# Performance work log

Hardware: AMD Instinct MI355X
Metric: run time of the kernel (lower is better)

The kernel has to match this reference:

```python
import jax, jax.numpy as jnp
import numpy as np

S = 64        # state_size (nodes per graph == feature width)
B = 1024      # number of graphs
N = B * S     # total nodes
DEG = 16      # avg degree
E = N * DEG   # total edges
A = 16        # attractors
EPS = 1e-5


def setup_inputs() -> dict:
    key = jax.random.key(0)
    ks = jax.random.split(key, 16)
    x = jax.random.normal(ks[0], (N, 1), dtype=jnp.float32)
    # block-diagonal batched graphs: each graph has S nodes, S*DEG edges
    epg = S * DEG
    gid = jnp.arange(E, dtype=jnp.int32) // epg
    src = gid * S + jax.random.randint(ks[1], (E,), 0, S, dtype=jnp.int32)
    dst = gid * S + jax.random.randint(ks[2], (E,), 0, S, dtype=jnp.int32)
    edge_index = jnp.stack([src, dst], axis=0)
    f32 = jnp.float32
    return {
        "x": x, "edge_index": edge_index,
        # EdgeConv MLP: Linear(2,4) -> ReLU -> Linear(4,S)
        "w1": jax.random.normal(ks[3], (2, 4), f32) * 0.5,
        "b1": jnp.zeros((4,), f32),
        "w2": jax.random.normal(ks[4], (4, S), f32) * 0.3,
        "b2": jnp.zeros((S,), f32),
        # Conv1d(S,S,3,padding=1) x2
        "conv2_w": jax.random.normal(ks[5], (S, S, 3), f32) / np.sqrt(3 * S),
        "conv2_b": jnp.zeros((S,), f32),
        "conv3_w": jax.random.normal(ks[6], (S, S, 3), f32) / np.sqrt(3 * S),
        "conv3_b": jnp.zeros((S,), f32),
        # BatchNorm affine params
        "g1": jnp.ones((S,), f32), "be1": jnp.zeros((S,), f32),
        "g2": jnp.ones((S,), f32), "be2": jnp.zeros((S,), f32),
        "g3": jnp.ones((S,), f32), "be3": jnp.zeros((S,), f32),
        # MLP tail
        "wm1": jax.random.normal(ks[7], (S * S, 256), f32) / np.sqrt(S * S),
        "bm1": jnp.zeros((256,), f32),
        "wm2": jax.random.normal(ks[8], (256, 256), f32) / 16.0,
        "bm2": jnp.zeros((256,), f32),
        "wm3": jax.random.normal(ks[9], (256, 256), f32) / 16.0,
        "bm3": jnp.zeros((256,), f32),
        "wp": jax.random.normal(ks[10], (256, A), f32) / 16.0,
        "bp": jnp.zeros((A,), f32),
    }


def _bn(h, gamma, beta, axes):
    # training-mode batch norm (biased variance), per-channel
    mean = jnp.mean(h, axis=axes, keepdims=True)
    var = jnp.mean(jnp.square(h - mean), axis=axes, keepdims=True)
    inv = jax.lax.rsqrt(var + EPS)
    sh = [1] * h.ndim
    sh[1] = -1
    return (h - mean) * inv * gamma.reshape(sh) + beta.reshape(sh)


def _conv1d(h, w, b):
    # h: [B, C, L], w: [O, I, K], padding=1 -> same length
    out = jax.lax.conv_general_dilated(
        h, w, window_strides=(1,), padding=((1, 1),),
        dimension_numbers=("NCH", "OIH", "NCH"))
    return out + b[None, :, None]


def reference(x, edge_index, w1, b1, w2, b2, conv2_w, conv2_b, conv3_w, conv3_b,
              g1, be1, g2, be2, g3, be3, wm1, bm1, wm2, bm2, wm3, bm3, wp, bp):
    src, dst = edge_index[0], edge_index[1]
    # EdgeConv (aggr='add'): nn(cat[x_i, x_j - x_i]) summed at target i
    xi = x[dst]                              # [E,1] gather
    xj = x[src]                              # [E,1] gather
    m = jnp.concatenate([xi, xj - xi], axis=-1)      # [E,2]
    m = jax.nn.relu(m @ w1 + b1)                     # [E,4]
    m = m @ w2 + b2                                   # [E,S]
    out = jax.ops.segment_sum(m, dst, num_segments=N)  # [N,S] scatter-add
    # BN1 + ReLU on [N,S] (channel dim = 1)
    out = jax.nn.relu(_bn(out, g1, be1, axes=(0,)))
    # per-graph feature map: [B, S_nodes, S_feat] -> channels-first [B,S,S]
    out = out.reshape(B, S, S).swapaxes(1, 2)
    out = jax.nn.relu(_bn(_conv1d(out, conv2_w, conv2_b), g2, be2, axes=(0, 2)))
    out = jax.nn.relu(_bn(_conv1d(out, conv3_w, conv3_b), g3, be3, axes=(0, 2)))
    out = out.reshape(B, S * S)
    out = jax.nn.relu(out @ wm1 + bm1)
    out = jax.nn.relu(out @ wm2 + bm2)
    out = jax.nn.relu(out @ wm3 + bm3)
    logits = out @ wp + bp                            # [B, A]
    return jax.nn.log_softmax(logits, axis=1)
```

## Files before the change

### kernel.cpp

```cpp
#include <hip/hip_runtime.h>
#include <cstdint>
#include <cstddef>

typedef __attribute__((ext_vector_type(8))) short short8;
typedef __attribute__((ext_vector_type(8))) unsigned short ushort8;
typedef __attribute__((ext_vector_type(4))) float f32x4;

#define EPSV 1e-5f
#define NB 1024
#define NEDGE 1048576
#define EPG 1024
#define CNTF 65536.0f
#define REP 32

__device__ __forceinline__ ushort f2bf(float f) {
  uint u = __float_as_uint(f);
  return (ushort)((u + 0x7FFFu + ((u >> 16) & 1u)) >> 16);
}
__device__ __forceinline__ float bf2f(ushort u) {
  return __uint_as_float((uint)u << 16);
}

__global__ __launch_bounds__(256) void k_prepw(
    const float* __restrict__ wm1, const float* __restrict__ wm2,
    const float* __restrict__ wm3, const float* __restrict__ wp,
    const float* __restrict__ c2w, const float* __restrict__ c3w,
    ushort* __restrict__ wbf1t, ushort* __restrict__ wbf2t,
    ushort* __restrict__ wbf3t, ushort* __restrict__ wptbf,
    ushort* __restrict__ cwt2, ushort* __restrict__ cwt3,
    float* __restrict__ stats)
{
  __shared__ ushort T[64][72];
  const int tid = threadIdx.x;
  const int bb = blockIdx.x;

  if (bb < 256) {
    const int kc = bb >> 2, n0 = (bb & 3) << 6;
    const int kk = tid >> 2, np = (tid & 3) << 4;
    const float* srow = wm1 + (((size_t)(kk << 6) + kc) << 8) + n0 + np;
#pragma unroll
    for (int i = 0; i < 4; ++i) {
      const float4 v = *(const float4*)(srow + (i << 2));
      const int n = np + (i << 2);
      T[n + 0][kk] = f2bf(v.x); T[n + 1][kk] = f2bf(v.y);
      T[n + 2][kk] = f2bf(v.z); T[n + 3][kk] = f2bf(v.w);
    }
    __syncthreads();
    ushort* dst = wbf1t + ((size_t)kc << 14) + (n0 << 6);
    const int nl = tid >> 2, qk = (tid & 3) << 4;
    *(ushort8*)(dst + (nl << 6) + qk) = *(ushort8*)&T[nl][qk];
    *(ushort8*)(dst + (nl << 6) + qk + 8) = *(ushort8*)&T[nl][qk + 8];
    return;
  }
  if (bb < 320) {
    const int base = (((bb - 256) << 8) + tid) << 3;
    const int m = base >> 16;
    const int rem = base & 65535;
    const int kc = rem >> 14, within = rem & 16383;
    const int n = within >> 6, kk0 = within & 63;
    const float* src = m ? wm3 : wm2;
    ushort* dst = m ? wbf3t : wbf2t;
    ushort tmp[8];
#pragma unroll
    for (int j = 0; j < 8; ++j)
      tmp[j] = f2bf(src[(((kc << 6) | (kk0 + j)) << 8) + n]);
    *(ushort8*)&dst[rem] = *(ushort8*)&tmp[0];
    return;
  }
  if (bb == 320) {
    const int a = tid & 15, k0 = (tid >> 4) << 4;
    ushort tmp[16];
#pragma unroll
    for (int j = 0; j < 16; ++j) tmp[j] = f2bf(wp[((k0 + j) << 4) + a]);
    *(ushort8*)&wptbf[(a << 8) + k0] = *(ushort8*)&tmp[0];
    *(ushort8*)&wptbf[(a << 8) + k0 + 8] = *(ushort8*)&tmp[8];
    return;
  }
  if (bb == 417) {
    float4 z4 = make_float4(0.f, 0.f, 0.f, 0.f);
#pragma unroll
    for (int i = 0; i < 12; ++i) ((float4*)stats)[(i << 8) + tid] = z4;
    return;
  }
  const int flat = (bb - 321) * 256 + tid;
  const int m = flat >= 12288;
  const int idx = flat - (m ? 12288 : 0);
  const float* src = m ? c3w : c2w;
  ushort* dst = m ? cwt3 : cwt2;
  const int o = idx / 192, rem = idx - o * 192;
  const int kk = rem >> 6, c = rem & 63;
  dst[idx] = f2bf(src[o * 192 + c * 3 + kk]);
}

__global__ __launch_bounds__(256) void k_edge(
    const float* __restrict__ x, const int* __restrict__ ei,
    const float* __restrict__ w1, const float* __restrict__ b1,
    const float* __restrict__ w2, const float* __restrict__ b2,
    ushort* __restrict__ out0, float* __restrict__ stats1)
{
  __shared__ float xs[64];
  __shared__ float aggT[4][5][72];
  __shared__ float aggC[64][8];
  __shared__ float w1s[8], b1s[4];
  __shared__ float w2s[256], b2s[64];
  __shared__ float rs[4][64], rss[4][64];
  const int tid = threadIdx.x;
  const int b = blockIdx.x;
  const int w = tid >> 6;

  if (tid < 8) w1s[tid] = w1[tid];
  if (tid < 4) b1s[tid] = b1[tid];
  if (tid < 64) { xs[tid] = x[(b << 6) + tid]; b2s[tid] = b2[tid]; }
  w2s[tid] = w2[tid];
  for (int i = tid; i < 1440; i += 256) ((float*)aggT)[i] = 0.f;
  __syncthreads();

  const int e0 = b * EPG;
  const int4 s4 = ((const int4*)(ei + e0))[tid];
  const int4 d4 = ((const int4*)(ei + NEDGE + e0))[tid];
  float* agw = &aggT[w][0][0];
  const int sls[4] = {s4.x & 63, s4.y & 63, s4.z & 63, s4.w & 63};
  const int dls[4] = {d4.x & 63, d4.y & 63, d4.z & 63, d4.w & 63};
#pragma unroll
  for (int e = 0; e < 4; ++e) {
    const int dl = dls[e];
    const float xi = xs[dl];
    const float dx = xs[sls[e]] - xi;
#pragma unroll
    for (int j = 0; j < 4; ++j) {
      float h = fmaxf(fmaf(xi, w1s[j], fmaf(dx, w1s[4 + j], b1s[j])), 0.f);
      atomicAdd(&agw[j * 72 + dl], h);
    }
    atomicAdd(&agw[4 * 72 + dl], 1.0f);
  }
  __syncthreads();

  if (tid < 64) {
    const int n = tid;
    const float a0 = aggT[0][0][n] + aggT[1][0][n] + aggT[2][0][n] + aggT[3][0][n];
    const float a1 = aggT[0][1][n] + aggT[1][1][n] + aggT[2][1][n] + aggT[3][1][n];
    const float a2 = aggT[0][2][n] + aggT[1][2][n] + aggT[2][2][n] + aggT[3][2][n];
    const float a3v = aggT[0][3][n] + aggT[1][3][n] + aggT[2][3][n] + aggT[3][3][n];
    const float dg = aggT[0][4][n] + aggT[1][4][n] + aggT[2][4][n] + aggT[3][4][n];
    *(float4*)&aggC[n][0] = make_float4(a0, a1, a2, a3v);
    aggC[n][4] = dg;
  }
  __syncthreads();

  const int c = tid & 63, qq = tid >> 6;
  const float wc0 = w2s[c], wc1 = w2s[64 + c], wc2 = w2s[128 + c], wc3 = w2s[192 + c];
  const float b2c = b2s[c];
  float s = 0.f, ss = 0.f;
  for (int n = qq; n < 64; n += 4) {
    const float4 a = *(const float4*)&aggC[n][0];
    const float dg = aggC[n][4];
    float v = a.x * wc0 + a.y * wc1 + a.z * wc2 + a.w * wc3 + dg * b2c;
    out0[(size_t)(((b << 6) + n) << 6) + c] = f2bf(v);
    s += v; ss += v * v;
  }
  rs[qq][c] = s; rss[qq][c] = ss;
  __syncthreads();
  if (tid < 64) {
    float* dst = stats1 + ((b & (REP - 1)) << 7);
    atomicAdd(&dst[tid], rs[0][tid] + rs[1][tid] + rs[2][tid] + rs[3][tid]);
    atomicAdd(&dst[64 + tid], rss[0][tid] + rss[1][tid] + rss[2][tid] + rss[3][tid]);
  }
}

__global__ __launch_bounds__(256) void k_convm(
    const ushort* __restrict__ in,
    const float* __restrict__ stats_in,
    const float* __restrict__ gamma, const float* __restrict__ beta,
    const ushort* __restrict__ cwt, const float* __restrict__ cb,
    ushort* __restrict__ out,
    float* __restrict__ stats_out)
{
  __shared__ ushort As[64][200];
  __shared__ ushort Yt[66][72];
  __shared__ float aco[64], bco[64], cbs[64];
  __shared__ float ldsS[64], ldsSS[64];
  const int tid = threadIdx.x;
  const int b = blockIdx.x;

  if (tid < 64) {
    float sm = 0.f, sq = 0.f;
#pragma unroll 8
    for (int r = 0; r < REP; ++r) {
      sm += stats_in[(r << 7) + tid];
      sq += stats_in[(r << 7) + 64 + tid];
    }
    const float mean = sm * (1.0f / CNTF);
    const float var = sq * (1.0f / CNTF) - mean * mean;
    const float a = gamma[tid] * rsqrtf(var + EPSV);
    aco[tid] = a;
    bco[tid] = beta[tid] - mean * a;
    cbs[tid] = cb[tid];
    Yt[0][tid] = 0;
    Yt[65][tid] = 0;
  }
  __syncthreads();

  const size_t base = (size_t)b << 12;
  {
    const int lr = tid >> 2, p = (tid & 3) << 4;
    const ushort8 r0 = *(const ushort8*)&in[base + (lr << 6) + p];
    const ushort8 r1 = *(const ushort8*)&in[base + (lr << 6) + p + 8];
    ushort tmp[16];
#pragma unroll
    for (int j = 0; j < 8; ++j)
      tmp[j] = f2bf(fmaxf(fmaf(aco[p + j], bf2f(r0[j]), bco[p + j]), 0.f));
#pragma unroll
    for (int j = 0; j < 8; ++j)
      tmp[8 + j] = f2bf(fmaxf(fmaf(aco[p + 8 + j], bf2f(r1[j]), bco[p + 8 + j]), 0.f));
    *(ushort8*)&Yt[lr + 1][p] = *(ushort8*)&tmp[0];
    *(ushort8*)&Yt[lr + 1][p + 8] = *(ushort8*)&tmp[8];
  }
  {
    const ushort8* gw = (const ushort8*)cwt;
#pragma unroll
    for (int i = 0; i < 6; ++i) {
      const int e8 = (i << 8) + tid;
      const int o = e8 / 24, k8 = (e8 - o * 24) << 3;
      *(ushort8*)&As[o][k8] = gw[e8];
    }
  }
  __syncthreads();

  const int lane = tid & 63, w = tid >> 6;
  const int lm = lane & 15, q = lane >> 4;
  f32x4 acc[4];
#pragma unroll
  for (int nt = 0; nt < 4; ++nt) acc[nt] = (f32x4){0.f, 0.f, 0.f, 0.f};

#pragma unroll
  for (int kk = 0; kk < 3; ++kk) {
#pragma unroll
    for (int ks = 0; ks < 2; ++ks) {
      const short8 af = *(const short8*)&As[(w << 4) + lm][(kk << 6) + (ks << 5) + (q << 3)];
#pragma unroll
      for (int nt = 0; nt < 4; ++nt) {
        const short8 bfr = *(const short8*)&Yt[(nt << 4) + lm + kk][(ks << 5) + (q << 3)];
        acc[nt] = __builtin_amdgcn_mfma_f32_16x16x32_bf16(af, bfr, acc[nt], 0, 0, 0);
      }
    }
  }

  const int obase = (w << 4) + (q << 2);
  const float4 cb4 = *(const float4*)&cbs[obase];
  float s[4] = {0.f, 0.f, 0.f, 0.f}, ss[4] = {0.f, 0.f, 0.f, 0.f};
#pragma unroll
  for (int nt = 0; nt < 4; ++nt) {
    const int l = (nt << 4) + lm;
    float4 v = make_float4(acc[nt][0] + cb4.x, acc[nt][1] + cb4.y,
                           acc[nt][2] + cb4.z, acc[nt][3] + cb4.w);
    *(ushort4*)&out[base + (l << 6) + obase] =
        make_ushort4(f2bf(v.x), f2bf(v.y), f2bf(v.z), f2bf(v.w));
    s[0] += v.x; ss[0] += v.x * v.x;
    s[1] += v.y; ss[1] += v.y * v.y;
    s[2] += v.z; ss[2] += v.z * v.z;
    s[3] += v.w; ss[3] += v.w * v.w;
  }
#pragma unroll
  for (int i = 0; i < 4; ++i) {
#pragma unroll
    for (int off = 1; off < 16; off <<= 1) {
      s[i] += __shfl_xor(s[i], off);
      ss[i] += __shfl_xor(ss[i], off);
    }
    if (lm == 0) { ldsS[obase + i] = s[i]; ldsSS[obase + i] = ss[i]; }
  }
  __syncthreads();
  if (tid < 64) {
    float* dst = stats_out + ((b & (REP - 1)) << 7);
    atomicAdd(&dst[tid], ldsS[tid]);
    atomicAdd(&dst[64 + tid], ldsSS[tid]);
  }
}

__global__ __launch_bounds__(256) void k_mlp1(
    const ushort* __restrict__ z3, const float* __restrict__ stats3,
    const float* __restrict__ g3, const float* __restrict__ be3,
    const ushort* __restrict__ wbf1t, float* __restrict__ h1part)
{
  __shared__ ushort Ys[64][72];
  __shared__ ushort Ws[128][72];
  __shared__ float a3s[64], b3s[64];
  const int tid = threadIdx.x;
  const int bx = blockIdx.x, by = blockIdx.y, bz = blockIdx.z;

  if (tid < 64) {
    float sm = 0.f, sq = 0.f;
#pragma unroll 8
    for (int r = 0; r < REP; ++r) {
      sm += stats3[(r << 7) + tid];
      sq += stats3[(r << 7) + 64 + tid];
    }
    const float mean = sm * (1.0f / CNTF);
    const float var = sq * (1.0f / CNTF) - mean * mean;
    const float a = g3[tid] * rsqrtf(var + EPSV);
    a3s[tid] = a;
    b3s[tid] = be3[tid] - mean * a;
  }
  __syncthreads();

  const int lane = tid & 63, w = tid >> 6;
  const int lm = lane & 15, q = lane >> 4;
  const int gy = tid >> 2, py = (tid & 3) << 4;
  const int nn = tid >> 1, pp = (tid & 1) << 2;
  const int g0 = bx << 6, n0 = by << 7;

  f32x4 acc[8];
#pragma unroll
  for (int nt = 0; nt < 8; ++nt) acc[nt] = (f32x4){0.f, 0.f, 0.f, 0.f};

  const size_t ybase = ((size_t)(g0 + gy) << 12);

#pragma unroll 1
  for (int ck = 0; ck < 8; ++ck) {
    const int kc = (bz << 9) + (ck << 6);
    if (ck) __syncthreads();
    {
      const ushort* src = z3 + ybase + kc + py;
      const ushort8 r0 = *(const ushort8*)src;
      const ushort8 r1 = *(const ushort8*)(src + 8);
      ushort tmp[16];
#pragma unroll
      for (int j = 0; j < 8; ++j)
        tmp[j] = f2bf(fmaxf(fmaf(a3s[py + j], bf2f(r0[j]), b3s[py + j]), 0.f));
#pragma unroll
      for (int j = 0; j < 8; ++j)
        tmp[8 + j] = f2bf(fmaxf(fmaf(a3s[py + 8 + j], bf2f(r1[j]), b3s[py + 8 + j]), 0.f));
      *(ushort8*)&Ys[gy][py] = *(ushort8*)&tmp[0];
      *(ushort8*)&Ys[gy][py + 8] = *(ushort8*)&tmp[8];
    }
    {
      const ushort8* gw = (const ushort8*)(wbf1t + ((size_t)((bz << 3) + ck) << 14) + (n0 << 6));
#pragma unroll
      for (int i = 0; i < 4; ++i)
        *(ushort8*)&Ws[nn][(pp + i) << 3] = gw[(nn << 3) + pp + i];
    }
    __syncthreads();
#pragma unroll
    for (int ks = 0; ks < 2; ++ks) {
      const short8 af = *(const short8*)&Ys[(w << 4) + lm][(ks << 5) + (q << 3)];
#pragma unroll
      for (int nt = 0; nt < 8; ++nt) {
        const short8 bfr = *(const short8*)&Ws[(nt << 4) + lm][(ks << 5) + (q << 3)];
        acc[nt] = __builtin_amdgcn_mfma_f32_16x16x32_bf16(af, bfr, acc[nt], 0, 0, 0);
      }
    }
  }

  float* dst0 = h1part + ((size_t)bz << 18);
  const int gout = g0 + (w << 4) + (q << 2);
#pragma unroll
  for (int nt = 0; nt < 8; ++nt) {
    const int col = n0 + (nt << 4) + lm;
#pragma unroll
    for (int i = 0; i < 4; ++i)
      dst0[((size_t)(gout + i) << 8) + col] = acc[nt][i];
  }
}

__global__ __launch_bounds__(256) void k_tail(
    const float* __restrict__ h1part, const float* __restrict__ bm1,
    const ushort* __restrict__ wbf2t, const float* __restrict__ bm2,
    const ushort* __restrict__ wbf3t, const float* __restrict__ bm3,
    const ushort* __restrict__ wptbf, const float* __restrict__ bp,
    float* __restrict__ out)
{
  __shared__ ushort Ws[256][72];
  __shared__ ushort h1s[16][264];
  __shared__ ushort h2s[16][264];
  ushort* wpt = &Ws[0][0];
  const int tid = threadIdx.x;
  const int g0 = blockIdx.x << 4;
  const int lane = tid & 63, w = tid >> 6;
  const int lm = lane & 15, q = lane >> 4;
  const int gr = q << 2;

  {
    const int r = tid >> 4, c0 = (tid & 15) << 4;
    const float* srcb = h1part + ((size_t)(g0 + r) << 8) + c0;
#pragma unroll
    for (int i = 0; i < 4; ++i) {
      float4 vs = *(const float4*)(bm1 + c0 + (i << 2));
#pragma unroll
      for (int bz = 0; bz < 8; ++bz) {
        const float4 p = *(const float4*)(srcb + ((size_t)bz << 18) + (i << 2));
        vs.x += p.x; vs.y += p.y; vs.z += p.z; vs.w += p.w;
      }
      *(ushort4*)&h1s[r][c0 + (i << 2)] = make_ushort4(
          f2bf(fmaxf(vs.x, 0.f)), f2bf(fmaxf(vs.y, 0.f)),
          f2bf(fmaxf(vs.z, 0.f)), f2bf(fmaxf(vs.w, 0.f)));
    }
  }

  f32x4 acc[4];
#pragma unroll
  for (int nt = 0; nt < 4; ++nt) acc[nt] = (f32x4){0.f, 0.f, 0.f, 0.f};
#pragma unroll 1
  for (int ck = 0; ck < 4; ++ck) {
    __syncthreads();
    {
      const ushort8* gw = (const ushort8*)(wbf2t + (ck << 14));
#pragma unroll
      for (int i = 0; i < 8; ++i) {
        const int e8 = (i << 8) + tid;
        const int n = e8 >> 3, kk = (e8 & 7) << 3;
        *(ushort8*)&Ws[n][kk] = gw[e8];
      }
    }
    __syncthreads();
#pragma unroll
    for (int ks = 0; ks < 2; ++ks) {
      const short8 af = *(const short8*)&h1s[lm][(ck << 6) + (ks << 5) + (q << 3)];
#pragma unroll
      for (int nt = 0; nt < 4; ++nt) {
        const short8 bfr = *(const short8*)&Ws[(w << 6) + (nt << 4) + lm][(ks << 5) + (q << 3)];
        acc[nt] = __builtin_amdgcn_mfma_f32_16x16x32_bf16(af, bfr, acc[nt], 0, 0, 0);
      }
    }
  }
#pragma unroll
  for (int nt = 0; nt < 4; ++nt) {
    const int col = (w << 6) + (nt << 4) + lm;
    const float bv = bm2[col];
#pragma unroll
    for (int i = 0; i < 4; ++i)
      h2s[gr + i][col] = f2bf(fmaxf(acc[nt][i] + bv, 0.f));
  }

  f32x4 acc2[4];
#pragma unroll
  for (int nt = 0; nt < 4; ++nt) acc2[nt] = (f32x4){0.f, 0.f, 0.f, 0.f};
#pragma unroll 1
  for (int ck = 0; ck < 4; ++ck) {
    __syncthreads();
    {
      const ushort8* gw = (const ushort8*)(wbf3t + (ck << 14));
#pragma unroll
      for (int i = 0; i < 8; ++i) {
        const int e8 = (i << 8) + tid;
        const int n = e8 >> 3, kk = (e8 & 7) << 3;
        *(ushort8*)&Ws[n][kk] = gw[e8];
      }
    }
    __syncthreads();
#pragma unroll
    for (int ks = 0; ks < 2; ++ks) {
      const short8 af = *(const short8*)&h2s[lm][(ck << 6) + (ks << 5) + (q << 3)];
#pragma unroll
      for (int nt = 0; nt < 4; ++nt) {
        const short8 bfr = *(const short8*)&Ws[(w << 6) + (nt << 4) + lm][(ks << 5) + (q << 3)];
        acc2[nt] = __builtin_amdgcn_mfma_f32_16x16x32_bf16(af, bfr, acc2[nt], 0, 0, 0);
      }
    }
  }

  __syncthreads();
  {
    const ushort8* gw = (const ushort8*)wptbf;
#pragma unroll
    for (int i = 0; i < 2; ++i) {
      const int e8 = (i << 8) + tid;
      const int flat = e8 << 3;
      const int a = flat >> 8, kk = flat & 255;
      *(ushort8*)&wpt[a * 264 + kk] = gw[e8];
    }
  }
#pragma unroll
  for (int nt = 0; nt < 4; ++nt) {
    const int col = (w << 6) + (nt << 4) + lm;
    const float bv = bm3[col];
#pragma unroll
    for (int i = 0; i < 4; ++i)
      h2s[gr + i][col] = f2bf(fmaxf(acc2[nt][i] + bv, 0.f));
  }
  __syncthreads();

  if (w == 0) {
    f32x4 lacc = (f32x4){0.f, 0.f, 0.f, 0.f};
#pragma unroll
    for (int ks = 0; ks < 8; ++ks) {
      const short8 af = *(const short8*)&h2s[lm][(ks << 5) + (q << 3)];
      const short8 bfr = *(const short8*)&wpt[lm * 264 + (ks << 5) + (q << 3)];
      lacc = __builtin_amdgcn_mfma_f32_16x16x32_bf16(af, bfr, lacc, 0, 0, 0);
    }
    const float bpv = bp[lm];
    float lg[4], mx[4], se[4];
#pragma unroll
    for (int i = 0; i < 4; ++i) {
      lg[i] = lacc[i] + bpv;
      float m = lg[i];
#pragma unroll
      for (int off = 1; off < 16; off <<= 1) m = fmaxf(m, __shfl_xor(m, off));
      mx[i] = m;
      float e = expf(lg[i] - m);
#pragma unroll
      for (int off = 1; off < 16; off <<= 1) e += __shfl_xor(e, off);
      se[i] = e;
    }
#pragma unroll
    for (int i = 0; i < 4; ++i)
      out[((g0 + gr + i) << 4) + lm] = (lg[i] - mx[i]) - logf(se[i]);
  }
}

extern "C" void kernel_launch(void* const* d_in, const int* in_sizes, int n_in,
                              void* d_out, int out_size, void* d_ws, size_t ws_size,
                              hipStream_t stream)
{
  const float* x   = (const float*)d_in[0];
  const int*   ei  = (const int*)d_in[1];
  const float* w1  = (const float*)d_in[2];
  const float* b1  = (const float*)d_in[3];
  const float* w2  = (const float*)d_in[4];
  const float* b2  = (const float*)d_in[5];
  const float* c2w = (const float*)d_in[6];
  const float* c2b = (const float*)d_in[7];
  const float* c3w = (const float*)d_in[8];
  const float* c3b = (const float*)d_in[9];
  const float* g1  = (const float*)d_in[10];
  const float* be1 = (const float*)d_in[11];
  const float* g2  = (const float*)d_in[12];
  const float* be2 = (const float*)d_in[13];
  const float* g3  = (const float*)d_in[14];
  const float* be3 = (const float*)d_in[15];
  const float* wm1 = (const float*)d_in[16];
  const float* bm1 = (const float*)d_in[17];
  const float* wm2 = (const float*)d_in[18];
  const float* bm2 = (const float*)d_in[19];
  const float* wm3 = (const float*)d_in[20];
  const float* bm3 = (const float*)d_in[21];
  const float* wp  = (const float*)d_in[22];
  const float* bp  = (const float*)d_in[23];

  char* ws = (char*)d_ws;
  ushort* ubuf0 = (ushort*)ws;
  ushort* ubuf1 = (ushort*)(ws + ((size_t)8 << 20));
  float*  h1part = (float*)(ws + ((size_t)16 << 20));
  ushort* wbf1t = (ushort*)(ws + ((size_t)24 << 20));
  ushort* wbf2t = (ushort*)(ws + ((size_t)26 << 20));
  ushort* wbf3t = (ushort*)(ws + ((size_t)26 << 20) + (128 << 10));
  ushort* wptbf = (ushort*)(ws + ((size_t)26 << 20) + (256 << 10));
  float* stats = (float*)(ws + ((size_t)27 << 20));
  float* stats1 = stats;
  float* stats2 = stats + REP * 128;
  float* stats3 = stats + 2 * REP * 128;
  ushort* cwt2 = (ushort*)d_out;
  ushort* cwt3 = (ushort*)d_out + 12288;

  k_prepw<<<dim3(418), dim3(256), 0, stream>>>(
      wm1, wm2, wm3, wp, c2w, c3w,
      wbf1t, wbf2t, wbf3t, wptbf, cwt2, cwt3, stats);
  k_edge<<<dim3(NB), dim3(256), 0, stream>>>(x, ei, w1, b1, w2, b2, ubuf0, stats1);
  k_convm<<<dim3(NB), dim3(256), 0, stream>>>(ubuf0, stats1, g1, be1, cwt2, c2b, ubuf1, stats2);
  k_convm<<<dim3(NB), dim3(256), 0, stream>>>(ubuf1, stats2, g2, be2, cwt3, c3b, ubuf0, stats3);
  k_mlp1<<<dim3(16, 2, 8), dim3(256), 0, stream>>>(ubuf0, stats3, g3, be3, wbf1t, h1part);
  k_tail<<<dim3(64), dim3(256), 0, stream>>>(h1part, bm1, wbf2t, bm2, wbf3t, bm3,
                                             wptbf, bp, (float*)d_out);
}
```

Measured before the change: 187.8 us.

## Fuse all stages into one persistent kernel with software grid barriers

Replaces six separate kernel launches with one persistent 256-block kernel. Stages are separated by atomic-counter grid barriers, blocks loop over graphs in a grid-stride pattern, and the stats zeroing moves to a memset. The aim is to remove launch gaps and tail effects between the small kernels. In exchange it relies on all 256 blocks being co-resident, adds spin-wait barrier overhead, and cuts parallelism from 1024 blocks to 256.

```diff
diff --git a/kernel.cpp b/kernel.cpp
--- a/kernel.cpp
+++ b/kernel.cpp
@@ -7,11 +7,11 @@
 typedef __attribute__((ext_vector_type(4))) float f32x4;
 
 #define EPSV 1e-5f
-#define NB 1024
 #define NEDGE 1048576
 #define EPG 1024
 #define CNTF 65536.0f
 #define REP 32
+#define GRID 256
 
 __device__ __forceinline__ ushort f2bf(float f) {
   uint u = __float_as_uint(f);
@@ -21,39 +21,198 @@
   return __uint_as_float((uint)u << 16);
 }
 
-__global__ __launch_bounds__(256) void k_prepw(
-    const float* __restrict__ wm1, const float* __restrict__ wm2,
-    const float* __restrict__ wm3, const float* __restrict__ wp,
+__device__ __forceinline__ void gbar(int* bar, int nb) {
+  __syncthreads();
+  if (threadIdx.x == 0) {
+    __threadfence();
+    __hip_atomic_fetch_add(bar, 1, __ATOMIC_ACQ_REL, __HIP_MEMORY_SCOPE_AGENT);
+    while (__hip_atomic_load(bar, __ATOMIC_ACQUIRE, __HIP_MEMORY_SCOPE_AGENT) < nb)
+      __builtin_amdgcn_s_sleep(1);
+    __threadfence();
+  }
+  __syncthreads();
+}
+
+struct SmemEdge {
+  float xs[64];
+  float aggT[4][5][72];
+  float aggC[64][8];
+  float w1s[8], b1s[4];
+  float w2s[256], b2s[64];
+  float rs[4][64], rss[4][64];
+};
+struct SmemPrep { ushort T[64][72]; };
+struct SmemConv {
+  ushort As[64][200];
+  ushort Yt[66][72];
+  float aco[64], bco[64], cbs[64];
+  float ldsS[64], ldsSS[64];
+};
+struct SmemMlp1 {
+  float a3s[64], b3s[64];
+  ushort Ys[64][72];
+  ushort Ws[128][72];
+};
+struct SmemTail {
+  ushort Ws[256][72];
+  ushort h1s[16][264];
+  ushort h2s[16][264];
+};
+
+__device__ __forceinline__ void conv_stage(
+    SmemConv* S, const int b, const int tid,
+    const ushort* __restrict__ in, const float* __restrict__ stats_in,
+    const float* __restrict__ gamma, const float* __restrict__ beta,
+    const ushort* __restrict__ cwt, const float* __restrict__ cb,
+    ushort* __restrict__ out, float* __restrict__ stats_out)
+{
+  if (tid < 64) {
+    float sm = 0.f, sq = 0.f;
+#pragma unroll 8
+    for (int r = 0; r < REP; ++r) {
+      sm += stats_in[(r << 7) + tid];
+      sq += stats_in[(r << 7) + 64 + tid];
+    }
+    const float mean = sm * (1.0f / CNTF);
+    const float var = sq * (1.0f / CNTF) - mean * mean;
+    const float a = gamma[tid] * rsqrtf(var + EPSV);
+    S->aco[tid] = a;
+    S->bco[tid] = beta[tid] - mean * a;
+    S->cbs[tid] = cb[tid];
+    S->Yt[0][tid] = 0;
+    S->Yt[65][tid] = 0;
+  }
+  {
+    const ushort8* gw = (const ushort8*)cwt;
+#pragma unroll
+    for (int i = 0; i < 6; ++i) {
+      const int e8 = (i << 8) + tid;
+      const int o = e8 / 24, k8 = (e8 - o * 24) << 3;
+      *(ushort8*)&S->As[o][k8] = gw[e8];
+    }
+  }
+  __syncthreads();
+
+  const int lane = tid & 63, w = tid >> 6;
+  const int lm = lane & 15, q = lane >> 4;
+
+#pragma unroll 1
+  for (int g = b; g < 1024; g += GRID) {
+    const size_t base = (size_t)g << 12;
+    {
+      const int lr = tid >> 2, p = (tid & 3) << 4;
+      const ushort8 r0 = *(const ushort8*)&in[base + (lr << 6) + p];
+      const ushort8 r1 = *(const ushort8*)&in[base + (lr << 6) + p + 8];
+      ushort tmp[16];
+#pragma unroll
+      for (int j = 0; j < 8; ++j)
+        tmp[j] = f2bf(fmaxf(fmaf(S->aco[p + j], bf2f(r0[j]), S->bco[p + j]), 0.f));
+#pragma unroll
+      for (int j = 0; j < 8; ++j)
+        tmp[8 + j] = f2bf(fmaxf(fmaf(S->aco[p + 8 + j], bf2f(r1[j]), S->bco[p + 8 + j]), 0.f));
+      *(ushort8*)&S->Yt[lr + 1][p] = *(ushort8*)&tmp[0];
+      *(ushort8*)&S->Yt[lr + 1][p + 8] = *(ushort8*)&tmp[8];
+    }
+    __syncthreads();
+
+    f32x4 acc[4];
+#pragma unroll
+    for (int nt = 0; nt < 4; ++nt) acc[nt] = (f32x4){0.f, 0.f, 0.f, 0.f};
+#pragma unroll
+    for (int kk = 0; kk < 3; ++kk) {
+#pragma unroll
+      for (int ks = 0; ks < 2; ++ks) {
+        const short8 af = *(const short8*)&S->As[(w << 4) + lm][(kk << 6) + (ks << 5) + (q << 3)];
+#pragma unroll
+        for (int nt = 0; nt < 4; ++nt) {
+          const short8 bfr = *(const short8*)&S->Yt[(nt << 4) + lm + kk][(ks << 5) + (q << 3)];
+          acc[nt] = __builtin_amdgcn_mfma_f32_16x16x32_bf16(af, bfr, acc[nt], 0, 0, 0);
+        }
+      }
+    }
+
+    const int obase = (w << 4) + (q << 2);
+    const float4 cb4 = *(const float4*)&S->cbs[obase];
+    float s[4] = {0.f, 0.f, 0.f, 0.f}, ss[4] = {0.f, 0.f, 0.f, 0.f};
+#pragma unroll
+    for (int nt = 0; nt < 4; ++nt) {
+      const int l = (nt << 4) + lm;
+      float4 v = make_float4(acc[nt][0] + cb4.x, acc[nt][1] + cb4.y,
+                             acc[nt][2] + cb4.z, acc[nt][3] + cb4.w);
+      *(ushort4*)&out[base + (l << 6) + obase] =
+          make_ushort4(f2bf(v.x), f2bf(v.y), f2bf(v.z), f2bf(v.w));
+      s[0] += v.x; ss[0] += v.x * v.x;
+      s[1] += v.y; ss[1] += v.y * v.y;
+      s[2] += v.z; ss[2] += v.z * v.z;
+      s[3] += v.w; ss[3] += v.w * v.w;
+    }
+#pragma unroll
+    for (int i = 0; i < 4; ++i) {
+#pragma unroll
+      for (int off = 1; off < 16; off <<= 1) {
+        s[i] += __shfl_xor(s[i], off);
+        ss[i] += __shfl_xor(ss[i], off);
+      }
+      if (lm == 0) { S->ldsS[obase + i] = s[i]; S->ldsSS[obase + i] = ss[i]; }
+    }
+    __syncthreads();
+    if (tid < 64) {
+      float* dst = stats_out + ((g & (REP - 1)) << 7);
+      atomicAdd(&dst[tid], S->ldsS[tid]);
+      atomicAdd(&dst[64 + tid], S->ldsSS[tid]);
+    }
+  }
+}
+
+__global__ __launch_bounds__(256, 2) void k_fused(
+    const float* __restrict__ x, const int* __restrict__ ei,
+    const float* __restrict__ w1, const float* __restrict__ b1,
+    const float* __restrict__ w2, const float* __restrict__ b2,
     const float* __restrict__ c2w, const float* __restrict__ c3w,
-    ushort* __restrict__ wbf1t, ushort* __restrict__ wbf2t,
-    ushort* __restrict__ wbf3t, ushort* __restrict__ wptbf,
+    const float* __restrict__ g1, const float* __restrict__ be1,
+    const float* __restrict__ c2b,
+    const float* __restrict__ g2, const float* __restrict__ be2,
+    const float* __restrict__ c3b,
+    const float* __restrict__ g3, const float* __restrict__ be3,
+    const float* __restrict__ wm1, const float* __restrict__ bm1,
+    const float* __restrict__ wm2, const float* __restrict__ bm2,
+    const float* __restrict__ wm3, const float* __restrict__ bm3,
+    const float* __restrict__ wp, const float* __restrict__ bp,
+    ushort* __restrict__ ubuf0, ushort* __restrict__ ubuf1,
+    float* __restrict__ h1part, ushort* __restrict__ wbf1t,
+    ushort* __restrict__ wbf2t, ushort* __restrict__ wbf3t,
+    ushort* __restrict__ wptbf, float* __restrict__ stats,
     ushort* __restrict__ cwt2, ushort* __restrict__ cwt3,
-    float* __restrict__ stats)
+    float* __restrict__ out, int* __restrict__ bar)
 {
-  __shared__ ushort T[64][72];
+  __shared__ __align__(16) char smem[sizeof(SmemTail)];
   const int tid = threadIdx.x;
-  const int bb = blockIdx.x;
-
-  if (bb < 256) {
-    const int kc = bb >> 2, n0 = (bb & 3) << 6;
+  const int b = blockIdx.x;
+  float* stats1 = stats;
+  float* stats2 = stats + REP * 128;
+  float* stats3 = stats + 2 * REP * 128;
+
+  {
+    SmemPrep* P = (SmemPrep*)smem;
+    const int kc = b >> 2, n0 = (b & 3) << 6;
     const int kk = tid >> 2, np = (tid & 3) << 4;
     const float* srow = wm1 + (((size_t)(kk << 6) + kc) << 8) + n0 + np;
 #pragma unroll
     for (int i = 0; i < 4; ++i) {
       const float4 v = *(const float4*)(srow + (i << 2));
       const int n = np + (i << 2);
-      T[n + 0][kk] = f2bf(v.x); T[n + 1][kk] = f2bf(v.y);
-      T[n + 2][kk] = f2bf(v.z); T[n + 3][kk] = f2bf(v.w);
+      P->T[n + 0][kk] = f2bf(v.x); P->T[n + 1][kk] = f2bf(v.y);
+      P->T[n + 2][kk] = f2bf(v.z); P->T[n + 3][kk] = f2bf(v.w);
     }
     __syncthreads();
     ushort* dst = wbf1t + ((size_t)kc << 14) + (n0 << 6);
     const int nl = tid >> 2, qk = (tid & 3) << 4;
-    *(ushort8*)(dst + (nl << 6) + qk) = *(ushort8*)&T[nl][qk];
-    *(ushort8*)(dst + (nl << 6) + qk + 8) = *(ushort8*)&T[nl][qk + 8];
-    return;
-  }
-  if (bb < 320) {
-    const int base = (((bb - 256) << 8) + tid) << 3;
+    *(ushort8*)(dst + (nl << 6) + qk) = *(ushort8*)&P->T[nl][qk];
+    *(ushort8*)(dst + (nl << 6) + qk + 8) = *(ushort8*)&P->T[nl][qk + 8];
+    __syncthreads();
+  }
+  if (b < 64) {
+    const int base = ((b << 8) + tid) << 3;
     const int m = base >> 16;
     const int rem = base & 65535;
     const int kc = rem >> 14, within = rem & 16383;
@@ -65,445 +224,310 @@
     for (int j = 0; j < 8; ++j)
       tmp[j] = f2bf(src[(((kc << 6) | (kk0 + j)) << 8) + n]);
     *(ushort8*)&dst[rem] = *(ushort8*)&tmp[0];
-    return;
-  }
-  if (bb == 320) {
+  } else if (b == 64) {
     const int a = tid & 15, k0 = (tid >> 4) << 4;
     ushort tmp[16];
 #pragma unroll
     for (int j = 0; j < 16; ++j) tmp[j] = f2bf(wp[((k0 + j) << 4) + a]);
     *(ushort8*)&wptbf[(a << 8) + k0] = *(ushort8*)&tmp[0];
     *(ushort8*)&wptbf[(a << 8) + k0 + 8] = *(ushort8*)&tmp[8];
-    return;
-  }
-  if (bb == 417) {
-    float4 z4 = make_float4(0.f, 0.f, 0.f, 0.f);
-#pragma unroll
-    for (int i = 0; i < 12; ++i) ((float4*)stats)[(i << 8) + tid] = z4;
-    return;
-  }
-  const int flat = (bb - 321) * 256 + tid;
-  const int m = flat >= 12288;
-  const int idx = flat - (m ? 12288 : 0);
-  const float* src = m ? c3w : c2w;
-  ushort* dst = m ? cwt3 : cwt2;
-  const int o = idx / 192, rem = idx - o * 192;
-  const int kk = rem >> 6, c = rem & 63;
-  dst[idx] = f2bf(src[o * 192 + c * 3 + kk]);
-}
-
-__global__ __launch_bounds__(256) void k_edge(
-    const float* __restrict__ x, const int* __restrict__ ei,
-    const float* __restrict__ w1, const float* __restrict__ b1,
-    const float* __restrict__ w2, const float* __restrict__ b2,
-    ushort* __restrict__ out0, float* __restrict__ stats1)
-{
-  __shared__ float xs[64];
-  __shared__ float aggT[4][5][72];
-  __shared__ float aggC[64][8];
-  __shared__ float w1s[8], b1s[4];
-  __shared__ float w2s[256], b2s[64];
-  __shared__ float rs[4][64], rss[4][64];
-  const int tid = threadIdx.x;
-  const int b = blockIdx.x;
-  const int w = tid >> 6;
-
-  if (tid < 8) w1s[tid] = w1[tid];
-  if (tid < 4) b1s[tid] = b1[tid];
-  if (tid < 64) { xs[tid] = x[(b << 6) + tid]; b2s[tid] = b2[tid]; }
-  w2s[tid] = w2[tid];
-  for (int i = tid; i < 1440; i += 256) ((float*)aggT)[i] = 0.f;
-  __syncthreads();
-
-  const int e0 = b * EPG;
-  const int4 s4 = ((const int4*)(ei + e0))[tid];
-  const int4 d4 = ((const int4*)(ei + NEDGE + e0))[tid];
-  float* agw = &aggT[w][0][0];
-  const int sls[4] = {s4.x & 63, s4.y & 63, s4.z & 63, s4.w & 63};
-  const int dls[4] = {d4.x & 63, d4.y & 63, d4.z & 63, d4.w & 63};
-#pragma unroll
-  for (int e = 0; e < 4; ++e) {
-    const int dl = dls[e];
-    const float xi = xs[dl];
-    const float dx = xs[sls[e]] - xi;
-#pragma unroll
-    for (int j = 0; j < 4; ++j) {
-      float h = fmaxf(fmaf(xi, w1s[j], fmaf(dx, w1s[4 + j], b1s[j])), 0.f);
-      atomicAdd(&agw[j * 72 + dl], h);
-    }
-    atomicAdd(&agw[4 * 72 + dl], 1.0f);
-  }
-  __syncthreads();
-
-  if (tid < 64) {
-    const int n = tid;
-    const float a0 = aggT[0][0][n] + aggT[1][0][n] + aggT[2][0][n] + aggT[3][0][n];
-    const float a1 = aggT[0][1][n] + aggT[1][1][n] + aggT[2][1][n] + aggT[3][1][n];
-    const float a2 = aggT[0][2][n] + aggT[1][2][n] + aggT[2][2][n] + aggT[3][2][n];
-    const float a3v = aggT[0][3][n] + aggT[1][3][n] + aggT[2][3][n] + aggT[3][3][n];
-    const float dg = aggT[0][4][n] + aggT[1][4][n] + aggT[2][4][n] + aggT[3][4][n];
-    *(float4*)&aggC[n][0] = make_float4(a0, a1, a2, a3v);
-    aggC[n][4] = dg;
-  }
-  __syncthreads();
-
-  const int c = tid & 63, qq = tid >> 6;
-  const float wc0 = w2s[c], wc1 = w2s[64 + c], wc2 = w2s[128 + c], wc3 = w2s[192 + c];
-  const float b2c = b2s[c];
-  float s = 0.f, ss = 0.f;
-  for (int n = qq; n < 64; n += 4) {
-    const float4 a = *(const float4*)&aggC[n][0];
-    const float dg = aggC[n][4];
-    float v = a.x * wc0 + a.y * wc1 + a.z * wc2 + a.w * wc3 + dg * b2c;
-    out0[(size_t)(((b << 6) + n) << 6) + c] = f2bf(v);
-    s += v; ss += v * v;
-  }
-  rs[qq][c] = s; rss[qq][c] = ss;
-  __syncthreads();
-  if (tid < 64) {
-    float* dst = stats1 + ((b & (REP - 1)) << 7);
-    atomicAdd(&dst[tid], rs[0][tid] + rs[1][tid] + rs[2][tid] + rs[3][tid]);
-    atomicAdd(&dst[64 + tid], rss[0][tid] + rss[1][tid] + rss[2][tid] + rss[3][tid]);
-  }
-}
-
-__global__ __launch_bounds__(256) void k_convm(
-    const ushort* __restrict__ in,
-    const float* __restrict__ stats_in,
-    const float* __restrict__ gamma, const float* __restrict__ beta,
-    const ushort* __restrict__ cwt, const float* __restrict__ cb,
-    ushort* __restrict__ out,
-    float* __restrict__ stats_out)
-{
-  __shared__ ushort As[64][200];
-  __shared__ ushort Yt[66][72];
-  __shared__ float aco[64], bco[64], cbs[64];
-  __shared__ float ldsS[64], ldsSS[64];
-  const int tid = threadIdx.x;
-  const int b = blockIdx.x;
-
-  if (tid < 64) {
-    float sm = 0.f, sq = 0.f;
+  } else if (b < 161) {
+    const int flat = (b - 65) * 256 + tid;
+    const int m = flat >= 12288;
+    const int idx = flat - (m ? 12288 : 0);
+    const float* src = m ? c3w : c2w;
+    ushort* dst = m ? cwt3 : cwt2;
+    const int o = idx / 192, rem2 = idx - o * 192;
+    const int kk = rem2 >> 6, c = rem2 & 63;
+    dst[idx] = f2bf(src[o * 192 + c * 3 + kk]);
+  }
+
+  {
+    SmemEdge* S = (SmemEdge*)smem;
+    const int w = tid >> 6;
+    if (tid < 8) S->w1s[tid] = w1[tid];
+    if (tid < 4) S->b1s[tid] = b1[tid];
+    if (tid < 64) S->b2s[tid] = b2[tid];
+    S->w2s[tid] = w2[tid];
+
+#pragma unroll 1
+    for (int g = b; g < 1024; g += GRID) {
+      if (tid < 64) S->xs[tid] = x[(g << 6) + tid];
+      for (int i = tid; i < 1440; i += 256) ((float*)S->aggT)[i] = 0.f;
+      __syncthreads();
+
+      const int e0 = g * EPG;
+      const int4 s4 = ((const int4*)(ei + e0))[tid];
+      const int4 d4 = ((const int4*)(ei + NEDGE + e0))[tid];
+      float* agw = &S->aggT[w][0][0];
+      const int sls[4] = {s4.x & 63, s4.y & 63, s4.z & 63, s4.w & 63};
+      const int dls[4] = {d4.x & 63, d4.y & 63, d4.z & 63, d4.w & 63};
+#pragma unroll
+      for (int e = 0; e < 4; ++e) {
+        const int dl = dls[e];
+        const float xi = S->xs[dl];
+        const float dx = S->xs[sls[e]] - xi;
+#pragma unroll
+        for (int j = 0; j < 4; ++j) {
+          float h = fmaxf(fmaf(xi, S->w1s[j], fmaf(dx, S->w1s[4 + j], S->b1s[j])), 0.f);
+          atomicAdd(&agw[j * 72 + dl], h);
+        }
+        atomicAdd(&agw[4 * 72 + dl], 1.0f);
+      }
+      __syncthreads();
+
+      if (tid < 64) {
+        const int n = tid;
+        const float a0 = S->aggT[0][0][n] + S->aggT[1][0][n] + S->aggT[2][0][n] + S->aggT[3][0][n];
+        const float a1 = S->aggT[0][1][n] + S->aggT[1][1][n] + S->aggT[2][1][n] + S->aggT[3][1][n];
+        const float a2 = S->aggT[0][2][n] + S->aggT[1][2][n] + S->aggT[2][2][n] + S->aggT[3][2][n];
+        const float a3v = S->aggT[0][3][n] + S->aggT[1][3][n] + S->aggT[2][3][n] + S->aggT[3][3][n];
+        const float dg = S->aggT[0][4][n] + S->aggT[1][4][n] + S->aggT[2][4][n] + S->aggT[3][4][n];
+        *(float4*)&S->aggC[n][0] = make_float4(a0, a1, a2, a3v);
+        S->aggC[n][4] = dg;
+      }
+      __syncthreads();
+
+      const int c = tid & 63, qq = tid >> 6;
+      const float wc0 = S->w2s[c], wc1 = S->w2s[64 + c];
+      const float wc2 = S->w2s[128 + c], wc3 = S->w2s[192 + c];
+      const float b2c = S->b2s[c];
+      float s = 0.f, ss = 0.f;
+      for (int n = qq; n < 64; n += 4) {
+        const float4 a = *(const float4*)&S->aggC[n][0];
+        const float dg = S->aggC[n][4];
+        float v = a.x * wc0 + a.y * wc1 + a.z * wc2 + a.w * wc3 + dg * b2c;
+        ubuf0[(size_t)(((g << 6) + n) << 6) + c] = f2bf(v);
+        s += v; ss += v * v;
+      }
+      S->rs[qq][c] = s; S->rss[qq][c] = ss;
+      __syncthreads();
+      if (tid < 64) {
+        float* dst = stats1 + ((g & (REP - 1)) << 7);
+        atomicAdd(&dst[tid], S->rs[0][tid] + S->rs[1][tid] + S->rs[2][tid] + S->rs[3][tid]);
+        atomicAdd(&dst[64 + tid], S->rss[0][tid] + S->rss[1][tid] + S->rss[2][tid] + S->rss[3][tid]);
+      }
+      __syncthreads();
+    }
+  }
+
+  gbar(bar + 0, GRID);
+  conv_stage((SmemConv*)smem, b, tid, ubuf0, stats1, g1, be1, cwt2, c2b, ubuf1, stats2);
+  gbar(bar + 16, GRID);
+  conv_stage((SmemConv*)smem, b, tid, ubuf1, stats2, g2, be2, cwt3, c3b, ubuf0, stats3);
+  gbar(bar + 32, GRID);
+
+  {
+    SmemMlp1* S = (SmemMlp1*)smem;
+    const int bx = b & 15, by = (b >> 4) & 1, bz = b >> 5;
+    if (tid < 64) {
+      float sm = 0.f, sq = 0.f;
 #pragma unroll 8
-    for (int r = 0; r < REP; ++r) {
-      sm += stats_in[(r << 7) + tid];
-      sq += stats_in[(r << 7) + 64 + tid];
-    }
-    const float mean = sm * (1.0f / CNTF);
-    const float var = sq * (1.0f / CNTF) - mean * mean;
-    const float a = gamma[tid] * rsqrtf(var + EPSV);
-    aco[tid] = a;
-    bco[tid] = beta[tid] - mean * a;
-    cbs[tid] = cb[tid];
-    Yt[0][tid] = 0;
-    Yt[65][tid] = 0;
-  }
-  __syncthreads();
-
-  const size_t base = (size_t)b << 12;
+      for (int r = 0; r < REP; ++r) {
+        sm += stats3[(r << 7) + tid];
+        sq += stats3[(r << 7) + 64 + tid];
+      }
+      const float mean = sm * (1.0f / CNTF);
+      const float var = sq * (1.0f / CNTF) - mean * mean;
+      const float a = g3[tid] * rsqrtf(var + EPSV);
+      S->a3s[tid] = a;
+      S->b3s[tid] = be3[tid] - mean * a;
+    }
+    __syncthreads();
+
+    const int lane = tid & 63, w = tid >> 6;
+    const int lm = lane & 15, q = lane >> 4;
+    const int gy = tid >> 2, py = (tid & 3) << 4;
+    const int nn = tid >> 1, pp = (tid & 1) << 2;
+    const int g0 = bx << 6, n0 = by << 7;
+
+    f32x4 acc[8];
+#pragma unroll
+    for (int nt = 0; nt < 8; ++nt) acc[nt] = (f32x4){0.f, 0.f, 0.f, 0.f};
+    const size_t ybase = ((size_t)(g0 + gy) << 12);
+
+#pragma unroll 1
+    for (int ck = 0; ck < 8; ++ck) {
+      const int kcg = (bz << 3) + ck;
+      const int kc = kcg << 6;
+      if (ck) __syncthreads();
+      {
+        const ushort* src = ubuf0 + ybase + kc + py;
+        const ushort8 r0 = *(const ushort8*)src;
+        const ushort8 r1 = *(const ushort8*)(src + 8);
+        ushort tmp[16];
+#pragma unroll
+        for (int j = 0; j < 8; ++j)
+          tmp[j] = f2bf(fmaxf(fmaf(S->a3s[py + j], bf2f(r0[j]), S->b3s[py + j]), 0.f));
+#pragma unroll
+        for (int j = 0; j < 8; ++j)
+          tmp[8 + j] = f2bf(fmaxf(fmaf(S->a3s[py + 8 + j], bf2f(r1[j]), S->b3s[py + 8 + j]), 0.f));
+        *(ushort8*)&S->Ys[gy][py] = *(ushort8*)&tmp[0];
+        *(ushort8*)&S->Ys[gy][py + 8] = *(ushort8*)&tmp[8];
+      }
+      {
+        const ushort8* gw = (const ushort8*)(wbf1t + ((size_t)kcg << 14) + (n0 << 6));
+#pragma unroll
+        for (int i = 0; i < 4; ++i)
+          *(ushort8*)&S->Ws[nn][(pp + i) << 3] = gw[(nn << 3) + pp + i];
+      }
+      __syncthreads();
+#pragma unroll
+      for (int ks = 0; ks < 2; ++ks) {
+        const short8 af = *(const short8*)&S->Ys[(w << 4) + lm][(ks << 5) + (q << 3)];
+#pragma unroll
+        for (int nt = 0; nt < 8; ++nt) {
+          const short8 bfr = *(const short8*)&S->Ws[(nt << 4) + lm][(ks << 5) + (q << 3)];
+          acc[nt] = __builtin_amdgcn_mfma_f32_16x16x32_bf16(af, bfr, acc[nt], 0, 0, 0);
+        }
+      }
+    }
+
+    float* dst0 = h1part + ((size_t)bz << 18);
+    const int gout = g0 + (w << 4) + (q << 2);
+#pragma unroll
+    for (int nt = 0; nt < 8; ++nt) {
+      const int col = n0 + (nt << 4) + lm;
+#pragma unroll
+      for (int i = 0; i < 4; ++i)
+        dst0[((size_t)(gout + i) << 8) + col] = acc[nt][i];
+    }
+  }
+
+  gbar(bar + 48, GRID);
+  if (b >= 64) return;
   {
-    const int lr = tid >> 2, p = (tid & 3) << 4;
-    const ushort8 r0 = *(const ushort8*)&in[base + (lr << 6) + p];
-    const ushort8 r1 = *(const ushort8*)&in[base + (lr << 6) + p + 8];
-    ushort tmp[16];
-#pragma unroll
-    for (int j = 0; j < 8; ++j)
-      tmp[j] = f2bf(fmaxf(fmaf(aco[p + j], bf2f(r0[j]), bco[p + j]), 0.f));
-#pragma unroll
-    for (int j = 0; j < 8; ++j)
-      tmp[8 + j] = f2bf(fmaxf(fmaf(aco[p + 8 + j], bf2f(r1[j]), bco[p + 8 + j]), 0.f));
-    *(ushort8*)&Yt[lr + 1][p] = *(ushort8*)&tmp[0];
-    *(ushort8*)&Yt[lr + 1][p + 8] = *(ushort8*)&tmp[8];
-  }
-  {
-    const ushort8* gw = (const ushort8*)cwt;
-#pragma unroll
-    for (int i = 0; i < 6; ++i) {
-      const int e8 = (i << 8) + tid;
-      const int o = e8 / 24, k8 = (e8 - o * 24) << 3;
-      *(ushort8*)&As[o][k8] = gw[e8];
-    }
-  }
-  __syncthreads();
-
-  const int lane = tid & 63, w = tid >> 6;
-  const int lm = lane & 15, q = lane >> 4;
-  f32x4 acc[4];
-#pragma unroll
-  for (int nt = 0; nt < 4; ++nt) acc[nt] = (f32x4){0.f, 0.f, 0.f, 0.f};
-
-#pragma unroll
-  for (int kk = 0; kk < 3; ++kk) {
-#pragma unroll
-    for (int ks = 0; ks < 2; ++ks) {
-      const short8 af = *(const short8*)&As[(w << 4) + lm][(kk << 6) + (ks << 5) + (q << 3)];
-#pragma unroll
-      for (int nt = 0; nt < 4; ++nt) {
-        const short8 bfr = *(const short8*)&Yt[(nt << 4) + lm + kk][(ks << 5) + (q << 3)];
-        acc[nt] = __builtin_amdgcn_mfma_f32_16x16x32_bf16(af, bfr, acc[nt], 0, 0, 0);
-      }
-    }
-  }
-
-  const int obase = (w << 4) + (q << 2);
-  const float4 cb4 = *(const float4*)&cbs[obase];
-  float s[4] = {0.f, 0.f, 0.f, 0.f}, ss[4] = {0.f, 0.f, 0.f, 0.f};
-#pragma unroll
-  for (int nt = 0; nt < 4; ++nt) {
-    const int l = (nt << 4) + lm;
-    float4 v = make_float4(acc[nt][0] + cb4.x, acc[nt][1] + cb4.y,
-                           acc[nt][2] + cb4.z, acc[nt][3] + cb4.w);
-    *(ushort4*)&out[base + (l << 6) + obase] =
-        make_ushort4(f2bf(v.x), f2bf(v.y), f2bf(v.z), f2bf(v.w));
-    s[0] += v.x; ss[0] += v.x * v.x;
-    s[1] += v.y; ss[1] += v.y * v.y;
-    s[2] += v.z; ss[2] += v.z * v.z;
-    s[3] += v.w; ss[3] += v.w * v.w;
-  }
-#pragma unroll
-  for (int i = 0; i < 4; ++i) {
-#pragma unroll
-    for (int off = 1; off < 16; off <<= 1) {
-      s[i] += __shfl_xor(s[i], off);
-      ss[i] += __shfl_xor(ss[i], off);
-    }
-    if (lm == 0) { ldsS[obase + i] = s[i]; ldsSS[obase + i] = ss[i]; }
-  }
-  __syncthreads();
-  if (tid < 64) {
-    float* dst = stats_out + ((b & (REP - 1)) << 7);
-    atomicAdd(&dst[tid], ldsS[tid]);
-    atomicAdd(&dst[64 + tid], ldsSS[tid]);
-  }
-}
-
-__global__ __launch_bounds__(256) void k_mlp1(
-    const ushort* __restrict__ z3, const float* __restrict__ stats3,
-    const float* __restrict__ g3, const float* __restrict__ be3,
-    const ushort* __restrict__ wbf1t, float* __restrict__ h1part)
-{
-  __shared__ ushort Ys[64][72];
-  __shared__ ushort Ws[128][72];
-  __shared__ float a3s[64], b3s[64];
-  const int tid = threadIdx.x;
-  const int bx = blockIdx.x, by = blockIdx.y, bz = blockIdx.z;
-
-  if (tid < 64) {
-    float sm = 0.f, sq = 0.f;
-#pragma unroll 8
-    for (int r = 0; r < REP; ++r) {
-      sm += stats3[(r << 7) + tid];
-      sq += stats3[(r << 7) + 64 + tid];
-    }
-    const float mean = sm * (1.0f / CNTF);
-    const float var = sq * (1.0f / CNTF) - mean * mean;
-    const float a = g3[tid] * rsqrtf(var + EPSV);
-    a3s[tid] = a;
-    b3s[tid] = be3[tid] - mean * a;
-  }
-  __syncthreads();
-
-  const int lane = tid & 63, w = tid >> 6;
-  const int lm = lane & 15, q = lane >> 4;
-  const int gy = tid >> 2, py = (tid & 3) << 4;
-  const int nn = tid >> 1, pp = (tid & 1) << 2;
-  const int g0 = bx << 6, n0 = by << 7;
-
-  f32x4 acc[8];
-#pragma unroll
-  for (int nt = 0; nt < 8; ++nt) acc[nt] = (f32x4){0.f, 0.f, 0.f, 0.f};
-
-  const size_t ybase = ((size_t)(g0 + gy) << 12);
-
+    SmemTail* S = (SmemTail*)smem;
+    ushort* wpt = &S->Ws[0][0];
+    const int g0 = b << 4;
+    const int lane = tid & 63, w = tid >> 6;
+    const int lm = lane & 15, q = lane >> 4;
+    const int gr = q << 2;
+
+    {
+      const int r = tid >> 4, c0 = (tid & 15) << 4;
+      const float* srcb = h1part + ((size_t)(g0 + r) << 8) + c0;
+#pragma unroll
+      for (int i = 0; i < 4; ++i) {
+        float4 vs = *(const float4*)(bm1 + c0 + (i << 2));
+#pragma unroll
+        for (int bz = 0; bz < 8; ++bz) {
+          const float4 p = *(const float4*)(srcb + ((size_t)bz << 18) + (i << 2));
+          vs.x += p.x; vs.y += p.y; vs.z += p.z; vs.w += p.w;
+        }
+        *(ushort4*)&S->h1s[r][c0 + (i << 2)] = make_ushort4(
+            f2bf(fmaxf(vs.x, 0.f)), f2bf(fmaxf(vs.y, 0.f)),
+            f2bf(fmaxf(vs.z, 0.f)), f2bf(fmaxf(vs.w, 0.f)));
+      }
+    }
+
+    f32x4 acc[4];
+#pragma unroll
+    for (int nt = 0; nt < 4; ++nt) acc[nt] = (f32x4){0.f, 0.f, 0.f, 0.f};
 #pragma unroll 1
-  for (int ck = 0; ck < 8; ++ck) {
-    const int kc = (bz << 9) + (ck << 6);
-    if (ck) __syncthreads();
+    for (int ck = 0; ck < 4; ++ck) {
+      __syncthreads();
+      {
+        const ushort8* gw = (const ushort8*)(wbf2t + (ck << 14));
+#pragma unroll
+        for (int i = 0; i < 8; ++i) {
+          const int e8 = (i << 8) + tid;
+          *(ushort8*)&S->Ws[e8 >> 3][(e8 & 7) << 3] = gw[e8];
+        }
+      }
+      __syncthreads();
+#pragma unroll
+      for (int ks = 0; ks < 2; ++ks) {
+        const short8 af = *(const short8*)&S->h1s[lm][(ck << 6) + (ks << 5) + (q << 3)];
+#pragma unroll
+        for (int nt = 0; nt < 4; ++nt) {
+          const short8 bfr = *(const short8*)&S->Ws[(w << 6) + (nt << 4) + lm][(ks << 5) + (q << 3)];
+          acc[nt] = __builtin_amdgcn_mfma_f32_16x16x32_bf16(af, bfr, acc[nt], 0, 0, 0);
+        }
+      }
+    }
+#pragma unroll
+    for (int nt = 0; nt < 4; ++nt) {
+      const int col = (w << 6) + (nt << 4) + lm;
+      const float bv = bm2[col];
+#pragma unroll
+      for (int i = 0; i < 4; ++i)
+        S->h2s[gr + i][col] = f2bf(fmaxf(acc[nt][i] + bv, 0.f));
+    }
+
+    f32x4 acc2[4];
+#pragma unroll
+    for (int nt = 0; nt < 4; ++nt) acc2[nt] = (f32x4){0.f, 0.f, 0.f, 0.f};
+#pragma unroll 1
+    for (int ck = 0; ck < 4; ++ck) {
+      __syncthreads();
+      {
+        const ushort8* gw = (const ushort8*)(wbf3t + (ck << 14));
+#pragma unroll
+        for (int i = 0; i < 8; ++i) {
+          const int e8 = (i << 8) + tid;
+          *(ushort8*)&S->Ws[e8 >> 3][(e8 & 7) << 3] = gw[e8];
+        }
+      }
+      __syncthreads();
+#pragma unroll
+      for (int ks = 0; ks < 2; ++ks) {
+        const short8 af = *(const short8*)&S->h2s[lm][(ck << 6) + (ks << 5) + (q << 3)];
+#pragma unroll
+        for (int nt = 0; nt < 4; ++nt) {
+          const short8 bfr = *(const short8*)&S->Ws[(w << 6) + (nt << 4) + lm][(ks << 5) + (q << 3)];
+          acc2[nt] = __builtin_amdgcn_mfma_f32_16x16x32_bf16(af, bfr, acc2[nt], 0, 0, 0);
+        }
+      }
+    }
+
+    __syncthreads();
     {
-      const ushort* src = z3 + ybase + kc + py;
-      const ushort8 r0 = *(const ushort8*)src;
-      const ushort8 r1 = *(const ushort8*)(src + 8);
-      ushort tmp[16];
-#pragma unroll
-      for (int j = 0; j < 8; ++j)
-        tmp[j] = f2bf(fmaxf(fmaf(a3s[py + j], bf2f(r0[j]), b3s[py + j]), 0.f));
-#pragma unroll
-      for (int j = 0; j < 8; ++j)
-        tmp[8 + j] = f2bf(fmaxf(fmaf(a3s[py + 8 + j], bf2f(r1[j]), b3s[py + 8 + j]), 0.f));
-      *(ushort8*)&Ys[gy][py] = *(ushort8*)&tmp[0];
-      *(ushort8*)&Ys[gy][py + 8] = *(ushort8*)&tmp[8];
-    }
-    {
-      const ushort8* gw = (const ushort8*)(wbf1t + ((size_t)((bz << 3) + ck) << 14) + (n0 << 6));
+      const ushort8* gw = (const ushort8*)wptbf;
+#pragma unroll
+      for (int i = 0; i < 2; ++i) {
+        const int e8 = (i << 8) + tid;
+        const int flat = e8 << 3;
+        const int a = flat >> 8, kk = flat & 255;
+        *(ushort8*)&wpt[a * 264 + kk] = gw[e8];
+      }
+    }
+#pragma unroll
+    for (int nt = 0; nt < 4; ++nt) {
+      const int col = (w << 6) + (nt << 4) + lm;
+      const float bv = bm3[col];
 #pragma unroll
       for (int i = 0; i < 4; ++i)
-        *(ushort8*)&Ws[nn][(pp + i) << 3] = gw[(nn << 3) + pp + i];
-    }
-    __syncthreads();
-#pragma unroll
-    for (int ks = 0; ks < 2; ++ks) {
-      const short8 af = *(const short8*)&Ys[(w << 4) + lm][(ks << 5) + (q << 3)];
-#pragma unroll
-      for (int nt = 0; nt < 8; ++nt) {
-        const short8 bfr = *(const short8*)&Ws[(nt << 4) + lm][(ks << 5) + (q << 3)];
-        acc[nt] = __builtin_amdgcn_mfma_f32_16x16x32_bf16(af, bfr, acc[nt], 0, 0, 0);
-      }
-    }
-  }
-
-  float* dst0 = h1part + ((size_t)bz << 18);
-  const int gout = g0 + (w << 4) + (q << 2);
-#pragma unroll
-  for (int nt = 0; nt < 8; ++nt) {
-    const int col = n0 + (nt << 4) + lm;
-#pragma unroll
-    for (int i = 0; i < 4; ++i)
-      dst0[((size_t)(gout + i) << 8) + col] = acc[nt][i];
-  }
-}
-
-__global__ __launch_bounds__(256) void k_tail(
-    const float* __restrict__ h1part, const float* __restrict__ bm1,
-    const ushort* __restrict__ wbf2t, const float* __restrict__ bm2,
-    const ushort* __restrict__ wbf3t, const float* __restrict__ bm3,
-    const ushort* __restrict__ wptbf, const float* __restrict__ bp,
-    float* __restrict__ out)
-{
-  __shared__ ushort Ws[256][72];
-  __shared__ ushort h1s[16][264];
-  __shared__ ushort h2s[16][264];
-  ushort* wpt = &Ws[0][0];
-  const int tid = threadIdx.x;
-  const int g0 = blockIdx.x << 4;
-  const int lane = tid & 63, w = tid >> 6;
-  const int lm = lane & 15, q = lane >> 4;
-  const int gr = q << 2;
-
-  {
-    const int r = tid >> 4, c0 = (tid & 15) << 4;
-    const float* srcb = h1part + ((size_t)(g0 + r) << 8) + c0;
-#pragma unroll
-    for (int i = 0; i < 4; ++i) {
-      float4 vs = *(const float4*)(bm1 + c0 + (i << 2));
-#pragma unroll
-      for (int bz = 0; bz < 8; ++bz) {
-        const float4 p = *(const float4*)(srcb + ((size_t)bz << 18) + (i << 2));
-        vs.x += p.x; vs.y += p.y; vs.z += p.z; vs.w += p.w;
-      }
-      *(ushort4*)&h1s[r][c0 + (i << 2)] = make_ushort4(
-          f2bf(fmaxf(vs.x, 0.f)), f2bf(fmaxf(vs.y, 0.f)),
-          f2bf(fmaxf(vs.z, 0.f)), f2bf(fmaxf(vs.w, 0.f)));
-    }
-  }
-
-  f32x4 acc[4];
-#pragma unroll
-  for (int nt = 0; nt < 4; ++nt) acc[nt] = (f32x4){0.f, 0.f, 0.f, 0.f};
-#pragma unroll 1
-  for (int ck = 0; ck < 4; ++ck) {
-    __syncthreads();
-    {
-      const ushort8* gw = (const ushort8*)(wbf2t + (ck << 14));
-#pragma unroll
-      for (int i = 0; i < 8; ++i) {
-        const int e8 = (i << 8) + tid;
-        const int n = e8 >> 3, kk = (e8 & 7) << 3;
-        *(ushort8*)&Ws[n][kk] = gw[e8];
-      }
-    }
-    __syncthreads();
-#pragma unroll
-    for (int ks = 0; ks < 2; ++ks) {
-      const short8 af = *(const short8*)&h1s[lm][(ck << 6) + (ks << 5) + (q << 3)];
-#pragma unroll
-      for (int nt = 0; nt < 4; ++nt) {
-        const short8 bfr = *(const short8*)&Ws[(w << 6) + (nt << 4) + lm][(ks << 5) + (q << 3)];
-        acc[nt] = __builtin_amdgcn_mfma_f32_16x16x32_bf16(af, bfr, acc[nt], 0, 0, 0);
-      }
-    }
-  }
-#pragma unroll
-  for (int nt = 0; nt < 4; ++nt) {
-    const int col = (w << 6) + (nt << 4) + lm;
-    const float bv = bm2[col];
-#pragma unroll
-    for (int i = 0; i < 4; ++i)
-      h2s[gr + i][col] = f2bf(fmaxf(acc[nt][i] + bv, 0.f));
-  }
-
-  f32x4 acc2[4];
-#pragma unroll
-  for (int nt = 0; nt < 4; ++nt) acc2[nt] = (f32x4){0.f, 0.f, 0.f, 0.f};
-#pragma unroll 1
-  for (int ck = 0; ck < 4; ++ck) {
-    __syncthreads();
-    {
-      const ushort8* gw = (const ushort8*)(wbf3t + (ck << 14));
-#pragma unroll
-      for (int i = 0; i < 8; ++i) {
-        const int e8 = (i << 8) + tid;
-        const int n = e8 >> 3, kk = (e8 & 7) << 3;
-        *(ushort8*)&Ws[n][kk] = gw[e8];
-      }
-    }
-    __syncthreads();
-#pragma unroll
-    for (int ks = 0; ks < 2; ++ks) {
-      const short8 af = *(const short8*)&h2s[lm][(ck << 6) + (ks << 5) + (q << 3)];
-#pragma unroll
-      for (int nt = 0; nt < 4; ++nt) {
-        const short8 bfr = *(const short8*)&Ws[(w << 6) + (nt << 4) + lm][(ks << 5) + (q << 3)];
-        acc2[nt] = __builtin_amdgcn_mfma_f32_16x16x32_bf16(af, bfr, acc2[nt], 0, 0, 0);
-      }
-    }
-  }
-
-  __syncthreads();
-  {
-    const ushort8* gw = (const ushort8*)wptbf;
-#pragma unroll
-    for (int i = 0; i < 2; ++i) {
-      const int e8 = (i << 8) + tid;
-      const int flat = e8 << 3;
-      const int a = flat >> 8, kk = flat & 255;
-      *(ushort8*)&wpt[a * 264 + kk] = gw[e8];
-    }
-  }
-#pragma unroll
-  for (int nt = 0; nt < 4; ++nt) {
-    const int col = (w << 6) + (nt << 4) + lm;
-    const float bv = bm3[col];
-#pragma unroll
-    for (int i = 0; i < 4; ++i)
-      h2s[gr + i][col] = f2bf(fmaxf(acc2[nt][i] + bv, 0.f));
-  }
-  __syncthreads();
-
-  if (w == 0) {
-    f32x4 lacc = (f32x4){0.f, 0.f, 0.f, 0.f};
-#pragma unroll
-    for (int ks = 0; ks < 8; ++ks) {
-      const short8 af = *(const short8*)&h2s[lm][(ks << 5) + (q << 3)];
-      const short8 bfr = *(const short8*)&wpt[lm * 264 + (ks << 5) + (q << 3)];
-      lacc = __builtin_amdgcn_mfma_f32_16x16x32_bf16(af, bfr, lacc, 0, 0, 0);
-    }
-    const float bpv = bp[lm];
-    float lg[4], mx[4], se[4];
-#pragma unroll
-    for (int i = 0; i < 4; ++i) {
-      lg[i] = lacc[i] + bpv;
-      float m = lg[i];
-#pragma unroll
-      for (int off = 1; off < 16; off <<= 1) m = fmaxf(m, __shfl_xor(m, off));
-      mx[i] = m;
-      float e = expf(lg[i] - m);
-#pragma unroll
-      for (int off = 1; off < 16; off <<= 1) e += __shfl_xor(e, off);
-      se[i] = e;
-    }
-#pragma unroll
-    for (int i = 0; i < 4; ++i)
-      out[((g0 + gr + i) << 4) + lm] = (lg[i] - mx[i]) - logf(se[i]);
+        S->h2s[gr + i][col] = f2bf(fmaxf(acc2[nt][i] + bv, 0.f));
+    }
+    __syncthreads();
+
+    if (w == 0) {
+      f32x4 lacc = (f32x4){0.f, 0.f, 0.f, 0.f};
+#pragma unroll
+      for (int ks = 0; ks < 8; ++ks) {
+        const short8 af = *(const short8*)&S->h2s[lm][(ks << 5) + (q << 3)];
+        const short8 bfr = *(const short8*)&wpt[lm * 264 + (ks << 5) + (q << 3)];
+        lacc = __builtin_amdgcn_mfma_f32_16x16x32_bf16(af, bfr, lacc, 0, 0, 0);
+      }
+      const float bpv = bp[lm];
+      float lg[4], mx[4], se[4];
+#pragma unroll
+      for (int i = 0; i < 4; ++i) {
+        lg[i] = lacc[i] + bpv;
+        float m = lg[i];
+#pragma unroll
+        for (int off = 1; off < 16; off <<= 1) m = fmaxf(m, __shfl_xor(m, off));
+        mx[i] = m;
+        float e = expf(lg[i] - m);
+#pragma unroll
+        for (int off = 1; off < 16; off <<= 1) e += __shfl_xor(e, off);
+        se[i] = e;
+      }
+#pragma unroll
+      for (int i = 0; i < 4; ++i)
+        out[((g0 + gr + i) << 4) + lm] = (lg[i] - mx[i]) - logf(se[i]);
+    }
   }
 }
 
@@ -544,20 +568,17 @@
   ushort* wbf2t = (ushort*)(ws + ((size_t)26 << 20));
   ushort* wbf3t = (ushort*)(ws + ((size_t)26 << 20) + (128 << 10));
   ushort* wptbf = (ushort*)(ws + ((size_t)26 << 20) + (256 << 10));
-  float* stats = (float*)(ws + ((size_t)27 << 20));
-  float* stats1 = stats;
-  float* stats2 = stats + REP * 128;
-  float* stats3 = stats + 2 * REP * 128;
+  float* stats  = (float*)(ws + ((size_t)27 << 20));
+  int*   bar    = (int*)(stats + 3 * REP * 128);
   ushort* cwt2 = (ushort*)d_out;
   ushort* cwt3 = (ushort*)d_out + 12288;
 
-  k_prepw<<<dim3(418), dim3(256), 0, stream>>>(
-      wm1, wm2, wm3, wp, c2w, c3w,
-      wbf1t, wbf2t, wbf3t, wptbf, cwt2, cwt3, stats);
-  k_edge<<<dim3(NB), dim3(256), 0, stream>>>(x, ei, w1, b1, w2, b2, ubuf0, stats1);
-  k_convm<<<dim3(NB), dim3(256), 0, stream>>>(ubuf0, stats1, g1, be1, cwt2, c2b, ubuf1, stats2);
-  k_convm<<<dim3(NB), dim3(256), 0, stream>>>(ubuf1, stats2, g2, be2, cwt3, c3b, ubuf0, stats3);
-  k_mlp1<<<dim3(16, 2, 8), dim3(256), 0, stream>>>(ubuf0, stats3, g3, be3, wbf1t, h1part);
-  k_tail<<<dim3(64), dim3(256), 0, stream>>>(h1part, bm1, wbf2t, bm2, wbf3t, bm3,
-                                             wptbf, bp, (float*)d_out);
+  hipMemsetAsync(stats, 0, 3 * REP * 128 * sizeof(float) + 64 * sizeof(int),
+                 stream);
+  k_fused<<<dim3(GRID), dim3(256), 0, stream>>>(
+      x, ei, w1, b1, w2, b2, c2w, c3w,
+      g1, be1, c2b, g2, be2, c3b, g3, be3,
+      wm1, bm1, wm2, bm2, wm3, bm3, wp, bp,
+      ubuf0, ubuf1, h1part, wbf1t, wbf2t, wbf3t, wptbf, stats,
+      cwt2, cwt3, (float*)d_out, bar);
 }
```

Measured after the change: 283.1 us. 50.7% more time.
